# Performance work log

Measured on AMD Instinct MI355X. Metric: run time of the kernel, lower is better.

The kernel has to match this reference:

```python
import jax, jax.numpy as jnp
import numpy as np

N_NODES = 100000
N_EDGES = 1600000
D = 128  # 2 * config.out_channels with config.out_channels = 64


def setup_inputs() -> dict:
    key = jax.random.key(0)
    k1, k2, k3, k4 = jax.random.split(key, 4)
    x_in = jax.random.normal(k1, (N_NODES, D), dtype=jnp.float32)
    x_out = jax.random.normal(k2, (N_NODES, D), dtype=jnp.float32)
    edge_index = jax.random.randint(k3, (2, N_EDGES), 0, N_NODES, dtype=jnp.int64)
    # nn.Bilinear(D, D, 1, bias=False) weight: [out_features=1, D, D]
    W = jax.random.normal(k4, (1, D, D), dtype=jnp.float32) * (1.0 / np.sqrt(D))
    return {"x_in": x_in, "x_out": x_out, "edge_index": edge_index, "W": W}


def reference(x_in, x_out, edge_index, W):
    # Gather edge endpoint features (irregular access)
    a = x_out[edge_index[0]]          # [E, D]
    b = x_in[edge_index[1]]           # [E, D]
    # Bilinear form with single output: value_e = a_e^T W0 b_e
    W0 = W[0]                         # [D, D]
    aW = a @ W0                       # [E, D]
    value = jnp.sum(aW * b, axis=-1)  # [E]
    return jax.nn.sigmoid(value)
```

## Files before the change

kernel.cpp:

```cpp
#include <hip/hip_runtime.h>
#include <hip/hip_fp16.h>
#include <math.h>

#define D 128
#define GM 64
#define CONV_BLOCKS 2048

typedef _Float16 f16x8 __attribute__((ext_vector_type(8)));
typedef float    f32x4 __attribute__((ext_vector_type(4)));
typedef _Float16 h2_t  __attribute__((ext_vector_type(2)));

__device__ __forceinline__ float dot2acc(unsigned ua, unsigned ub, float c) {
#if __has_builtin(__builtin_amdgcn_fdot2)
  return __builtin_amdgcn_fdot2(__builtin_bit_cast(h2_t, ua),
                                __builtin_bit_cast(h2_t, ub), c, false);
#else
  __half2 a = __builtin_bit_cast(__half2, ua);
  __half2 b = __builtin_bit_cast(__half2, ub);
  float2 fa = __half22float2(a), fb = __half22float2(b);
  return fmaf(fa.x, fb.x, fmaf(fa.y, fb.y, c));
#endif
}

__device__ __forceinline__ unsigned pack2(float x, float y) {
  __half2 h;
  h.x = __float2half_rn(x);
  h.y = __float2half_rn(y);
  return __builtin_bit_cast(unsigned, h);
}

__global__ __launch_bounds__(256) void prep3_kernel(
    const float* __restrict__ Xout, const float* __restrict__ Xin,
    const float* __restrict__ W, __half* __restrict__ Yh,
    __half* __restrict__ Xh, int N, int gemm_blocks)
{
  __shared__ __align__(16) __half sA[GM * D];
  __shared__ __align__(16) __half sB[D * D];

  const int tid = threadIdx.x;
  const int bid = blockIdx.x;

  if (bid >= gemm_blocks) {
    const int cb = bid - gemm_blocks;
    const int n4 = N * (D / 4);
    const int stride = CONV_BLOCKS * 256 * 4;
    for (int base = (cb * 256 + tid) * 4; base < n4; base += stride) {
      float4 v[4];
      #pragma unroll
      for (int j = 0; j < 4; j++)
        if (base + j < n4) v[j] = ((const float4*)Xin)[base + j];
      #pragma unroll
      for (int j = 0; j < 4; j++)
        if (base + j < n4) {
          uint2 u;
          u.x = pack2(v[j].x, v[j].y);
          u.y = pack2(v[j].z, v[j].w);
          ((uint2*)Xh)[base + j] = u;
        }
    }
    return;
  }

  const int row0 = bid * GM;

  float4 v[8];
  #pragma unroll
  for (int i = 0; i < 4; i++) {
    int gi = tid + i * 256;
    int r = gi >> 4, q = gi & 15;
    int gr = row0 + r;
    if (gr < N) {
      const float4* s = (const float4*)(Xout + (size_t)gr * D + q * 8);
      v[2*i]   = s[0];
      v[2*i+1] = s[1];
    } else {
      v[2*i]   = make_float4(0.f, 0.f, 0.f, 0.f);
      v[2*i+1] = make_float4(0.f, 0.f, 0.f, 0.f);
    }
  }
  #pragma unroll
  for (int i = 0; i < 4; i++) {
    int gi = tid + i * 256;
    int r = gi >> 4, q = gi & 15;
    uint4 u;
    u.x = pack2(v[2*i].x,   v[2*i].y);
    u.y = pack2(v[2*i].z,   v[2*i].w);
    u.z = pack2(v[2*i+1].x, v[2*i+1].y);
    u.w = pack2(v[2*i+1].z, v[2*i+1].w);
    *(uint4*)(sA + r * D + ((q ^ (r & 7)) << 3)) = u;
  }

  #pragma unroll
  for (int i = 0; i < 64; i++) {
    int o = tid + i * 256;
    int k = o >> 7;
    int n = o & 127;
    __half h = __float2half_rn(W[o]);
    int gk = k >> 3;
    sB[n * 128 + (((gk + n) & 15) << 3) + (k & 7)] = h;
  }
  __syncthreads();

  const int lane = tid & 63, wave = tid >> 6;
  const int m = lane & 15, quad = lane >> 4;
  const int rloc = wave * 16 + m;

  f32x4 acc[8];
  #pragma unroll
  for (int ct = 0; ct < 8; ct++) acc[ct] = (f32x4){0.f, 0.f, 0.f, 0.f};

  #pragma unroll
  for (int ks = 0; ks < 4; ks++) {
    const int g = ks * 4 + quad;
    f16x8 bfrag[8];
    #pragma unroll
    for (int ct = 0; ct < 8; ct++) {
      int n = ct * 16 + m;
      bfrag[ct] = *(const f16x8*)(sB + n * 128 + (((g + n) & 15) << 3));
    }
    f16x8 afrag = *(const f16x8*)(sA + rloc * D + ((g ^ (rloc & 7)) << 3));
    #pragma unroll
    for (int ct = 0; ct < 8; ct++)
      acc[ct] = __builtin_amdgcn_mfma_f32_16x16x32_f16(
          afrag, bfrag[ct], acc[ct], 0, 0, 0);
  }

  __syncthreads();
  __half* sC = sA;
  #pragma unroll
  for (int ct = 0; ct < 8; ct++)
    #pragma unroll
    for (int reg = 0; reg < 4; reg++) {
      int r = wave * 16 + quad * 4 + reg;
      sC[r * D + ct * 16 + m] = __float2half_rn(acc[ct][reg]);
    }
  __syncthreads();
  #pragma unroll
  for (int i = 0; i < 4; i++) {
    int gi = tid + i * 256;
    int r = gi >> 4, q = gi & 15;
    int gr = row0 + r;
    if (gr < N)
      *(uint4*)(Yh + (size_t)gr * D + q * 8) = *(const uint4*)(sC + r * D + q * 8);
  }
}

__global__ __launch_bounds__(256) void edge_dot2_kernel(
    const __half* __restrict__ Yh, const __half* __restrict__ Xh,
    const int* __restrict__ idx, float* __restrict__ out, int E)
{
  long long gid = (long long)blockIdx.x * 256 + threadIdx.x;
  int slot = (int)(gid >> 4);
  int l    = (int)(gid & 15);
  int e0 = slot * 2;
  if (e0 >= E) return;
  int e1 = e0 + 1;
  bool has1 = (e1 < E);

  int s0 = idx[e0];
  int d0 = idx[E + e0];
  int s1 = has1 ? idx[e1] : s0;
  int d1 = has1 ? idx[E + e1] : d0;

  uint4 a0 = ((const uint4*)(Yh + (size_t)s0 * D))[l];
  uint4 b0 = ((const uint4*)(Xh + (size_t)d0 * D))[l];
  uint4 a1 = ((const uint4*)(Yh + (size_t)s1 * D))[l];
  uint4 b1 = ((const uint4*)(Xh + (size_t)d1 * D))[l];

  float p = 0.f, q = 0.f;
  p = dot2acc(a0.x, b0.x, p);  q = dot2acc(a1.x, b1.x, q);
  p = dot2acc(a0.y, b0.y, p);  q = dot2acc(a1.y, b1.y, q);
  p = dot2acc(a0.z, b0.z, p);  q = dot2acc(a1.z, b1.z, q);
  p = dot2acc(a0.w, b0.w, p);  q = dot2acc(a1.w, b1.w, q);

  p += __shfl_xor(p, 8);  q += __shfl_xor(q, 8);
  p += __shfl_xor(p, 4);  q += __shfl_xor(q, 4);
  p += __shfl_xor(p, 2);  q += __shfl_xor(q, 2);
  p += __shfl_xor(p, 1);  q += __shfl_xor(q, 1);

  if (l == 0) {
    float2 o;
    o.x = 1.0f / (1.0f + __expf(-p));
    o.y = 1.0f / (1.0f + __expf(-q));
    if (has1) *(float2*)(out + e0) = o;
    else      out[e0] = o.x;
  }
}

__global__ __launch_bounds__(256) void edge_bilinear_direct_kernel(
    const float* __restrict__ Xout, const float* __restrict__ Xin,
    const float* __restrict__ W, const int* __restrict__ idx,
    float* __restrict__ out, int E)
{
  long long gid = (long long)blockIdx.x * 256 + threadIdx.x;
  int e = (int)(gid >> 6);
  if (e >= E) return;
  int l = (int)(gid & 63);

  int src = idx[e];
  int dst = idx[E + e];
  const float* a = Xout + (size_t)src * D;
  const float* b = Xin  + (size_t)dst * D;

  float s = 0.f;
  #pragma unroll
  for (int kk = 0; kk < 2; kk++) {
    int k = l + kk * 64;
    float ak = a[k];
    float t = 0.f;
    #pragma unroll 8
    for (int j = 0; j < D; j++) t = fmaf(W[(size_t)k * D + j], b[j], t);
    s = fmaf(ak, t, s);
  }
  #pragma unroll
  for (int off = 32; off >= 1; off >>= 1) s += __shfl_xor(s, off);
  if (l == 0) out[e] = 1.0f / (1.0f + __expf(-s));
}

extern "C" void kernel_launch(void* const* d_in, const int* in_sizes, int n_in,
                              void* d_out, int out_size, void* d_ws, size_t ws_size,
                              hipStream_t stream) {
  const float* x_in  = (const float*)d_in[0];
  const float* x_out = (const float*)d_in[1];
  const int*   eidx  = (const int*)d_in[2];
  const float* W     = (const float*)d_in[3];
  float* out = (float*)d_out;

  const int N = in_sizes[0] / D;
  const int E = in_sizes[2] / 2;

  const size_t half_rows = (size_t)N * D * sizeof(__half);

  if (ws_size >= 2 * half_rows) {
    __half* Yh = (__half*)d_ws;
    __half* Xh = (__half*)((char*)d_ws + half_rows);

    int gemm_blocks = (N + GM - 1) / GM;
    dim3 g1(gemm_blocks + CONV_BLOCKS);
    prep3_kernel<<<g1, 256, 0, stream>>>(x_out, x_in, W, Yh, Xh, N, gemm_blocks);

    long long slots = ((long long)E + 1) / 2;
    long long total = slots * 16;
    dim3 g2((unsigned)((total + 255) / 256));
    edge_dot2_kernel<<<g2, 256, 0, stream>>>(Yh, Xh, eidx, out, E);
  } else {
    long long total = (long long)E * 64;
    dim3 g((unsigned)((total + 255) / 256));
    edge_bilinear_direct_kernel<<<g, 256, 0, stream>>>(x_out, x_in, W, eidx, out, E);
  }
}
```

Measured before the change: 247.2 us.

## Bin edges by source/destination node range to improve gather locality

Adds a scatter pass that buckets each chunk of 8192 edges into 64 bins keyed by coarse source and destination node ranges. The edge kernel then walks the bins in bin-major order across chunks, so concurrently processed edges touch a narrower slice of Yh and Xh and can hit in cache. The cost is an extra kernel launch, about 1.6M index reads and writes for the permuted (src,dst) pairs and edge ids, and scattered output stores through the permutation. Each bin still spans roughly 12.5k nodes of each table (about 3.2MB per half table), so the reuse it gains is uncertain.

Result: slower. 298.0 us (+20.6%).

```diff
diff --git a/kernel.cpp b/kernel.cpp
--- a/kernel.cpp
+++ b/kernel.cpp
@@ -5,6 +5,8 @@
 #define D 128
 #define GM 64
 #define CONV_BLOCKS 2048
+#define EPB 8192
+#define EDGE_WGS 1024
 
 typedef _Float16 f16x8 __attribute__((ext_vector_type(8)));
 typedef float    f32x4 __attribute__((ext_vector_type(4)));
@@ -27,6 +29,69 @@
   h.x = __float2half_rn(x);
   h.y = __float2half_rn(y);
   return __builtin_bit_cast(unsigned, h);
+}
+
+__global__ __launch_bounds__(256) void scatter_kernel(
+    const int* __restrict__ eidx, int E, int N,
+    int2* __restrict__ sSD, int* __restrict__ sE,
+    int2* __restrict__ runs)
+{
+  __shared__ int2 sd[EPB];
+  __shared__ int  se[EPB];
+  __shared__ int  hist[64];
+  __shared__ int  base[64];
+  __shared__ int  cur[64];
+
+  const int tid = threadIdx.x;
+  const int b   = blockIdx.x;
+  const int e0  = b * EPB;
+  const int cnt = min(EPB, E - e0);
+  const float scale = 8.0f / (float)N;
+
+  for (int i = tid; i < 64; i += 256) hist[i] = 0;
+  __syncthreads();
+
+  int myk[EPB / 256];
+  #pragma unroll
+  for (int j = 0; j < EPB / 256; j++) {
+    int i = tid + j * 256;
+    if (i < cnt) {
+      int s = eidx[e0 + i];
+      int d = eidx[E + e0 + i];
+      int bs = min(7, (int)((float)s * scale));
+      int bd = min(7, (int)((float)d * scale));
+      int k = bs * 8 + bd;
+      myk[j] = k;
+      atomicAdd(&hist[k], 1);
+    } else myk[j] = -1;
+  }
+  __syncthreads();
+
+  if (tid == 0) {
+    int acc = 0;
+    for (int k = 0; k < 64; k++) { base[k] = acc; cur[k] = acc; acc += hist[k]; }
+  }
+  __syncthreads();
+
+  #pragma unroll
+  for (int j = 0; j < EPB / 256; j++) {
+    int i = tid + j * 256;
+    if (myk[j] >= 0) {
+      int s = eidx[e0 + i];
+      int d = eidx[E + e0 + i];
+      int pos = atomicAdd(&cur[myk[j]], 1);
+      sd[pos] = make_int2(s, d);
+      se[pos] = e0 + i;
+    }
+  }
+  __syncthreads();
+
+  for (int i = tid; i < cnt; i += 256) {
+    sSD[e0 + i] = sd[i];
+    sE[e0 + i]  = se[i];
+  }
+  for (int k = tid; k < 64; k += 256)
+    runs[b * 64 + k] = make_int2(e0 + base[k], hist[k]);
 }
 
 __global__ __launch_bounds__(256) void prep3_kernel(
@@ -145,6 +210,51 @@
   }
 }
 
+__global__ __launch_bounds__(256) void edge_binned_kernel(
+    const __half* __restrict__ Yh, const __half* __restrict__ Xh,
+    const int2* __restrict__ sSD, const int* __restrict__ sE,
+    const int2* __restrict__ runs, float* __restrict__ out, int NB)
+{
+  const int NP = NB * 64;
+  const int grp = threadIdx.x >> 4;
+  const int l   = threadIdx.x & 15;
+
+  for (int p = blockIdx.x; p < NP; p += gridDim.x) {
+    int bin = p / NB;
+    int b   = p - bin * NB;
+    int2 run = runs[b * 64 + bin];
+    int start = run.x, len = run.y;
+
+    for (int off = grp * 2; off < len; off += 32) {
+      int i0 = start + off;
+      bool has1 = (off + 1 < len);
+      int2 sd0 = sSD[i0];
+      int2 sd1 = has1 ? sSD[i0 + 1] : sd0;
+
+      uint4 a0 = ((const uint4*)(Yh + (size_t)sd0.x * D))[l];
+      uint4 b0 = ((const uint4*)(Xh + (size_t)sd0.y * D))[l];
+      uint4 a1 = ((const uint4*)(Yh + (size_t)sd1.x * D))[l];
+      uint4 b1 = ((const uint4*)(Xh + (size_t)sd1.y * D))[l];
+
+      float pv = 0.f, qv = 0.f;
+      pv = dot2acc(a0.x, b0.x, pv);  qv = dot2acc(a1.x, b1.x, qv);
+      pv = dot2acc(a0.y, b0.y, pv);  qv = dot2acc(a1.y, b1.y, qv);
+      pv = dot2acc(a0.z, b0.z, pv);  qv = dot2acc(a1.z, b1.z, qv);
+      pv = dot2acc(a0.w, b0.w, pv);  qv = dot2acc(a1.w, b1.w, qv);
+
+      pv += __shfl_xor(pv, 8);  qv += __shfl_xor(qv, 8);
+      pv += __shfl_xor(pv, 4);  qv += __shfl_xor(qv, 4);
+      pv += __shfl_xor(pv, 2);  qv += __shfl_xor(qv, 2);
+      pv += __shfl_xor(pv, 1);  qv += __shfl_xor(qv, 1);
+
+      if (l == 0) {
+        out[sE[i0]] = 1.0f / (1.0f + __expf(-pv));
+        if (has1) out[sE[i0 + 1]] = 1.0f / (1.0f + __expf(-qv));
+      }
+    }
+  }
+}
+
 __global__ __launch_bounds__(256) void edge_dot2_kernel(
     const __half* __restrict__ Yh, const __half* __restrict__ Xh,
     const int* __restrict__ idx, float* __restrict__ out, int E)
@@ -230,8 +340,31 @@
   const int E = in_sizes[2] / 2;
 
   const size_t half_rows = (size_t)N * D * sizeof(__half);
-
-  if (ws_size >= 2 * half_rows) {
+  const int NB = (E + EPB - 1) / EPB;
+
+  size_t off_yh  = 0;
+  size_t off_xh  = off_yh + half_rows;
+  size_t off_sd  = off_xh + half_rows;
+  size_t off_se  = off_sd + (size_t)E * sizeof(int2);
+  size_t off_rn  = off_se + (size_t)E * sizeof(int);
+  size_t total_ws = off_rn + (size_t)NB * 64 * sizeof(int2);
+
+  if (ws_size >= total_ws) {
+    __half* Yh   = (__half*)((char*)d_ws + off_yh);
+    __half* Xh   = (__half*)((char*)d_ws + off_xh);
+    int2*   sSD  = (int2*)((char*)d_ws + off_sd);
+    int*    sE   = (int*)((char*)d_ws + off_se);
+    int2*   runs = (int2*)((char*)d_ws + off_rn);
+
+    scatter_kernel<<<dim3(NB), 256, 0, stream>>>(eidx, E, N, sSD, sE, runs);
+
+    int gemm_blocks = (N + GM - 1) / GM;
+    dim3 g1(gemm_blocks + CONV_BLOCKS);
+    prep3_kernel<<<g1, 256, 0, stream>>>(x_out, x_in, W, Yh, Xh, N, gemm_blocks);
+
+    edge_binned_kernel<<<dim3(EDGE_WGS), 256, 0, stream>>>(Yh, Xh, sSD, sE,
+                                                           runs, out, NB);
+  } else if (ws_size >= 2 * half_rows) {
     __half* Yh = (__half*)d_ws;
     __half* Xh = (__half*)((char*)d_ws + half_rows);
 
```
